# Kernel tuning notes

Hardware: AMD Instinct MI355X
Metric: run time of the kernel (lower is better)

Reference implementation:

```python
import jax, jax.numpy as jnp
import numpy as np

DIM = 64      # channels
HEADS = 2     # num_heads -> head_dim = 32
K = 7         # neighborhood kernel_size (hardcoded in module)
B, H, W = 1, 96, 96
STAGES = 3
HEAD_DIM = DIM // HEADS


def setup_inputs() -> dict:
    key = jax.random.key(0)
    ks = jax.random.split(key, 6)
    x = jax.random.normal(ks[0], (B, DIM, H, W), jnp.float32)
    qkv_w = jax.random.normal(ks[1], (STAGES, 3 * DIM, DIM), jnp.float32) * 0.02
    qkv_b = jnp.zeros((STAGES, 3 * DIM), jnp.float32)
    proj_w = jax.random.normal(ks[2], (STAGES, DIM, DIM), jnp.float32) * 0.02
    proj_b = jnp.zeros((STAGES, DIM), jnp.float32)
    rpb = jax.random.normal(ks[3], (STAGES, HEADS, 2 * K - 1, 2 * K - 1), jnp.float32) * 0.02
    return {"x": x, "qkv_w": qkv_w, "qkv_b": qkv_b, "proj_w": proj_w,
            "proj_b": proj_b, "rpb": rpb}


def _window_idx(n):
    # NATTEN-style clamped sliding windows: each query attends to exactly K keys.
    starts = jnp.clip(jnp.arange(n) - K // 2, 0, n - K)
    idx = starts[:, None] + jnp.arange(K)          # [n, K] absolute key positions
    rel = idx - jnp.arange(n)[:, None] + (K - 1)   # [n, K] rpb index in [0, 2K-2]
    return idx, rel


def _na_stage(x, qkv_w, qkv_b, proj_w, proj_b, rpb, prev_attn):
    # x: [B, H, W, C]
    b, h_, w_, c = x.shape
    qkv = x @ qkv_w.T + qkv_b                                    # [B,H,W,3C]
    qkv = qkv.reshape(b, h_, w_, 3, HEADS, HEAD_DIM)
    qkv = jnp.transpose(qkv, (3, 0, 4, 1, 2, 5))                 # [3,B,h,H,W,d]
    q, k, v = qkv[0], qkv[1], qkv[2]
    scale = HEAD_DIM ** -0.5

    idx_h, rel_h = _window_idx(h_)
    idx_w, rel_w = _window_idx(w_)

    def gather_nb(t):  # t: [B,h,H,W,d] -> [B,h,H,W,K*K,d]
        t = t[:, :, idx_h]                       # [B,h,H,K,W,d]
        t = t[:, :, :, :, idx_w]                 # [B,h,H,K,W,K,d]
        t = jnp.transpose(t, (0, 1, 2, 4, 3, 5, 6))  # [B,h,H,W,K,K,d]
        return t.reshape(b, HEADS, h_, w_, K * K, HEAD_DIM)

    k_nb = gather_nb(k)
    v_nb = gather_nb(v)

    attn = jnp.einsum('bhijd,bhijkd->bhijk', q * scale, k_nb)   # [B,h,H,W,K*K]

    # relative positional bias: rpb[head, rel_h, rel_w]
    bias = rpb[:, rel_h[:, :, None, None], rel_w[None, None, :, :]]  # [h,H,K,W,K]
    bias = jnp.transpose(bias, (0, 1, 3, 2, 4)).reshape(HEADS, h_, w_, K * K)
    attn = attn + bias[None]

    if prev_attn is not None:  # high-order chaining: previous attention map added to logits
        attn = attn + prev_attn

    attn = jax.nn.softmax(attn, axis=-1)
    out = jnp.einsum('bhijk,bhijkd->bhijd', attn, v_nb)          # [B,h,H,W,d]
    out = jnp.transpose(out, (0, 2, 3, 1, 4)).reshape(b, h_, w_, c)
    out = out @ proj_w.T + proj_b
    return out, attn


def reference(x, qkv_w, qkv_b, proj_w, proj_b, rpb):
    xh = jnp.transpose(x, (0, 2, 3, 1))  # NCHW -> NHWC
    attn = None
    for s in range(STAGES):
        xh, attn = _na_stage(xh, qkv_w[s], qkv_b[s], proj_w[s], proj_b[s], rpb[s], attn)
    return jnp.transpose(xh, (0, 3, 1, 2))  # NHWC -> NCHW
```

## Files before the change

kernel.cpp:

```cpp
#include <hip/hip_runtime.h>

#define HW 96
#define NPIX 9216
#define QN 192
#define SCALE 0.17677669529663687f
#define NT 576

__device__ __forceinline__ int xswz(int row, int col) {
    return row * 64 + (((col & 60) ^ (((row >> 2) & 7) << 2)) | (col & 3));
}
__device__ __forceinline__ int wswz(int row, int col) {
    return row * 64 + (((col & 60) ^ ((row & 7) << 2)) | (col & 3));
}

template <int PAT>
__device__ __forceinline__ float swzf(float v) {
    return __int_as_float(__builtin_amdgcn_ds_swizzle(__float_as_int(v), PAT));
}

template <int N>
struct PVChain {
    static __device__ __forceinline__ void run(const float* __restrict__ vbase,
                                               const float* __restrict__ wk,
                                               float& a0, float& a1, float& c0, float& c1) {
        PVChain<N - 1>::run(vbase, wk, a0, a1, c0, c1);
        constexpr int kn = N >> 4, ln = N & 15;
        constexpr int av = N / 7, bv = N % 7;
        float w = __int_as_float(__builtin_amdgcn_ds_swizzle(
                      __float_as_int(wk[kn]), (ln << 5) | 0x10));
        const float2 v = *(const float2*)(vbase + (av * HW + bv) * QN);
        if (N & 1) { c0 = fmaf(w, v.x, c0); c1 = fmaf(w, v.y, c1); }
        else       { a0 = fmaf(w, v.x, a0); a1 = fmaf(w, v.y, a1); }
    }
};
template <>
struct PVChain<-1> {
    static __device__ __forceinline__ void run(const float*, const float*,
                                               float&, float&, float&, float&) {}
};

__device__ __forceinline__ void qkv_gemm(const float* __restrict__ xs,
                                         const float* __restrict__ ws,
                                         const float* __restrict__ qb,
                                         float* __restrict__ qkv,
                                         int i0, int j0c, int t)
{
    const int pxg = t % 9, jo = t / 9;
    const int jb = jo * 3;
    float acc[2][3];
    #pragma unroll
    for (int jj = 0; jj < 3; ++jj) {
        float bv = qb[jb + jj];
        acc[0][jj] = bv; acc[1][jj] = bv;
    }
    #pragma unroll
    for (int cc = 0; cc < 16; ++cc) {
        float4 xv[2], wv[3];
        #pragma unroll
        for (int ii = 0; ii < 2; ++ii)
            xv[ii] = *(const float4*)&xs[xswz(pxg * 2 + ii, cc * 4)];
        #pragma unroll
        for (int jj = 0; jj < 3; ++jj)
            wv[jj] = *(const float4*)&ws[wswz(jb + jj, cc * 4)];
        #pragma unroll
        for (int ii = 0; ii < 2; ++ii)
            #pragma unroll
            for (int jj = 0; jj < 3; ++jj) {
                acc[ii][jj] = fmaf(xv[ii].x, wv[jj].x, acc[ii][jj]);
                acc[ii][jj] = fmaf(xv[ii].y, wv[jj].y, acc[ii][jj]);
                acc[ii][jj] = fmaf(xv[ii].z, wv[jj].z, acc[ii][jj]);
                acc[ii][jj] = fmaf(xv[ii].w, wv[jj].w, acc[ii][jj]);
            }
    }
    #pragma unroll
    for (int ii = 0; ii < 2; ++ii) {
        int px = pxg * 2 + ii;
        float* o = qkv + ((i0 + px / 3) * HW + j0c + px % 3) * QN + jb;
        o[0] = acc[ii][0]; o[1] = acc[ii][1]; o[2] = acc[ii][2];
    }
}

__global__ __launch_bounds__(NT) void k_qkv0(const float* __restrict__ x,
                                             const float* __restrict__ qw,
                                             const float* __restrict__ qb,
                                             float* __restrict__ qkv)
{
    __shared__ float xs[18 * 64];
    __shared__ float ws[QN * 64];
    const int t = threadIdx.x;
    const int i0 = (blockIdx.x >> 5) * 6, j0c = (blockIdx.x & 31) * 3;
    #pragma unroll
    for (int it = 0; it < 2; ++it) {
        int l = it * NT + t;
        int px = l % 18, c = l / 18;
        xs[xswz(px, c)] = x[c * NPIX + (i0 + px / 3) * HW + j0c + px % 3];
    }
    #pragma unroll
    for (int it = 0; it < 6; ++it) {
        int l = it * NT + t;
        if (l < 3072) {
            int j = l >> 4, cs = (l & 15) << 2;
            *(float4*)&ws[wswz(j, cs)] = *(const float4*)&qw[j * 64 + cs];
        }
    }
    __syncthreads();
    qkv_gemm(xs, ws, qb, qkv, i0, j0c, t);
}

template <int HASPREV, int LAST>
__global__ __launch_bounds__(NT) void k_stage(const float* __restrict__ qkv,
                                              const float* __restrict__ rpb,
                                              const float* __restrict__ prev,
                                              float* __restrict__ cur,
                                              const float* __restrict__ pw,
                                              const float* __restrict__ pb,
                                              const float* __restrict__ qw,
                                              const float* __restrict__ qb,
                                              float* __restrict__ qkvn,
                                              float* __restrict__ outp)
{
    __shared__ float xs[18 * 64];
    __shared__ float ws[QN * 64];
    const int t = threadIdx.x;
    const int i0 = (blockIdx.x >> 5) * 6, j0c = (blockIdx.x & 31) * 3;
    #pragma unroll
    for (int it = 0; it < 2; ++it) {
        int l = it * NT + t;
        if (l < 1024) {
            int j = l >> 4, cs = (l & 15) << 2;
            *(float4*)&ws[wswz(j, cs)] = *(const float4*)&pw[j * 64 + cs];
        }
    }
    const int r = t & 15, g = t >> 4;
    const int h = g & 1, pl = g >> 1;
    const int i = i0 + pl / 3, jx = j0c + pl % 3;
    const int p = i * HW + jx;
    int si = i - 3;  si = si < 0 ? 0 : (si > 89 ? 89 : si);
    int sj = jx - 3; sj = sj < 0 ? 0 : (sj > 89 ? 89 : sj);
    float4 q[8];
    {
        const float4* qp = (const float4*)(qkv + p * QN + h * 32);
        #pragma unroll
        for (int d = 0; d < 8; ++d) q[d] = qp[d];
    }
    float pr[4] = {0.f, 0.f, 0.f, 0.f};
    if (HASPREV) {
        float4 z = *(const float4*)(prev + (p * 2 + h) * 64 + r * 4);
        pr[0] = z.x; pr[1] = z.y; pr[2] = z.z; pr[3] = z.w;
    }
    const float* kbase = qkv + (si * HW + sj) * QN + 64 + h * 32;
    float lg[4];
    int aa[4], bb[4];
    #pragma unroll
    for (int k = 0; k < 4; ++k) {
        int n = (k << 4) | r;
        int a = (n * 147) >> 10;
        int b = n - a * 7;
        aa[k] = a; bb[k] = b;
        const float4* kp = (const float4*)(kbase + (a * HW + b) * QN);
        float s0 = 0.f, s1 = 0.f, s2 = 0.f, s3 = 0.f;
        #pragma unroll
        for (int d = 0; d < 8; ++d) {
            float4 kv = kp[d];
            s0 = fmaf(q[d].x, kv.x, s0);
            s1 = fmaf(q[d].y, kv.y, s1);
            s2 = fmaf(q[d].z, kv.z, s2);
            s3 = fmaf(q[d].w, kv.w, s3);
        }
        lg[k] = (s0 + s1) + (s2 + s3);
    }
    {
        const float* rp = rpb + h * 169;
        const int rh0 = si - i + 6, rw0 = sj - jx + 6;
        #pragma unroll
        for (int k = 0; k < 4; ++k) {
            int n = (k << 4) | r;
            float v = fmaf(lg[k], SCALE, rp[(rh0 + aa[k]) * 13 + rw0 + bb[k]] + pr[k]);
            lg[k] = (n <= 48) ? v : -1e30f;
        }
    }
    float mx = fmaxf(fmaxf(lg[0], lg[1]), fmaxf(lg[2], lg[3]));
    mx = fmaxf(mx, swzf<0x041F>(mx));
    mx = fmaxf(mx, swzf<0x081F>(mx));
    mx = fmaxf(mx, swzf<0x101F>(mx));
    mx = fmaxf(mx, swzf<0x201F>(mx));
    float wk[4];
    float sum = 0.f;
    #pragma unroll
    for (int k = 0; k < 4; ++k) { wk[k] = expf(lg[k] - mx); sum += wk[k]; }
    sum += swzf<0x041F>(sum);
    sum += swzf<0x081F>(sum);
    sum += swzf<0x101F>(sum);
    sum += swzf<0x201F>(sum);
    const float inv = 1.f / sum;
    wk[0] *= inv; wk[1] *= inv; wk[2] *= inv; wk[3] *= inv;
    if (!LAST)
        *(float4*)(cur + (p * 2 + h) * 64 + r * 4) = make_float4(wk[0], wk[1], wk[2], wk[3]);
    {
        const float* vbase = qkv + (si * HW + sj) * QN + 128 + h * 32 + r * 2;
        float a0 = 0.f, a1 = 0.f, c0 = 0.f, c1 = 0.f;
        PVChain<48>::run(vbase, wk, a0, a1, c0, c1);
        *(float2*)&xs[xswz(pl, h * 32 + r * 2)] = make_float2(a0 + c0, a1 + c1);
    }
    __syncthreads();
    const int pxg = t % 9, jo = t / 9;
    float pa0 = pb[jo], pa1 = pa0;
    #pragma unroll
    for (int cc = 0; cc < 16; ++cc) {
        float4 xv0 = *(const float4*)&xs[xswz(pxg * 2, cc * 4)];
        float4 xv1 = *(const float4*)&xs[xswz(pxg * 2 + 1, cc * 4)];
        float4 wv  = *(const float4*)&ws[wswz(jo, cc * 4)];
        pa0 = fmaf(xv0.x, wv.x, pa0); pa0 = fmaf(xv0.y, wv.y, pa0);
        pa0 = fmaf(xv0.z, wv.z, pa0); pa0 = fmaf(xv0.w, wv.w, pa0);
        pa1 = fmaf(xv1.x, wv.x, pa1); pa1 = fmaf(xv1.y, wv.y, pa1);
        pa1 = fmaf(xv1.z, wv.z, pa1); pa1 = fmaf(xv1.w, wv.w, pa1);
    }
    __syncthreads();
    xs[xswz(pxg * 2, jo)]     = pa0;
    xs[xswz(pxg * 2 + 1, jo)] = pa1;
    if (!LAST) {
        #pragma unroll
        for (int it = 0; it < 6; ++it) {
            int l = it * NT + t;
            if (l < 3072) {
                int j = l >> 4, cs = (l & 15) << 2;
                *(float4*)&ws[wswz(j, cs)] = *(const float4*)&qw[j * 64 + cs];
            }
        }
    }
    __syncthreads();
    if (LAST) {
        #pragma unroll
        for (int it = 0; it < 2; ++it) {
            int l = it * NT + t;
            int px = l % 18, c = l / 18;
            outp[c * NPIX + (i0 + px / 3) * HW + j0c + px % 3] = xs[xswz(px, c)];
        }
        return;
    }
    qkv_gemm(xs, ws, qb, qkvn, i0, j0c, t);
}

extern "C" void kernel_launch(void* const* d_in, const int* in_sizes, int n_in,
                              void* d_out, int out_size, void* d_ws, size_t ws_size,
                              hipStream_t stream)
{
    const float* x   = (const float*)d_in[0];
    const float* qw  = (const float*)d_in[1];
    const float* qb  = (const float*)d_in[2];
    const float* pw  = (const float*)d_in[3];
    const float* pb  = (const float*)d_in[4];
    const float* rpb = (const float*)d_in[5];
    float* out = (float*)d_out;
    float* ws  = (float*)d_ws;

    float* qkvA = ws;
    float* qkvB = qkvA + 1769472;
    float* attA = qkvB + 1769472;
    float* attB = attA + 1179648;

    k_qkv0<<<512, NT, 0, stream>>>(x, qw, qb, qkvA);
    k_stage<0, 0><<<512, NT, 0, stream>>>(qkvA, rpb,       nullptr, attA,
                                          pw,        pb,       qw + 12288, qb + 192, qkvB, nullptr);
    k_stage<1, 0><<<512, NT, 0, stream>>>(qkvB, rpb + 338, attA,    attB,
                                          pw + 4096, pb + 64,  qw + 24576, qb + 384, qkvA, nullptr);
    k_stage<1, 1><<<512, NT, 0, stream>>>(qkvA, rpb + 676, attB,    nullptr,
                                          pw + 8192, pb + 128, nullptr,    nullptr,  nullptr, out);
}
```

Baseline: 185.7 us.

## Stage Q and attention weights in LDS, compact attention map stride

Loads Q for the block cooperatively into shared memory and computes the four logits per lane in one interleaved loop over head-dim chunks. Softmax weights go to an LDS buffer, which replaces the ds_swizzle broadcast chain in the PV product, and the stored attention map shrinks from 64 to 52 floats per pixel-head. Shuffles replace ds_swizzle for the reductions, and the launch bounds gain an occupancy hint. This adds LDS usage and an extra barrier but cuts global traffic for the prev/cur attention maps and register pressure.

```diff
diff --git a/kernel.cpp b/kernel.cpp
--- a/kernel.cpp
+++ b/kernel.cpp
@@ -3,6 +3,7 @@
 #define HW 96
 #define NPIX 9216
 #define QN 192
+#define ASTRIDE 52
 #define SCALE 0.17677669529663687f
 #define NT 576
 
@@ -12,32 +13,6 @@
 __device__ __forceinline__ int wswz(int row, int col) {
     return row * 64 + (((col & 60) ^ ((row & 7) << 2)) | (col & 3));
 }
-
-template <int PAT>
-__device__ __forceinline__ float swzf(float v) {
-    return __int_as_float(__builtin_amdgcn_ds_swizzle(__float_as_int(v), PAT));
-}
-
-template <int N>
-struct PVChain {
-    static __device__ __forceinline__ void run(const float* __restrict__ vbase,
-                                               const float* __restrict__ wk,
-                                               float& a0, float& a1, float& c0, float& c1) {
-        PVChain<N - 1>::run(vbase, wk, a0, a1, c0, c1);
-        constexpr int kn = N >> 4, ln = N & 15;
-        constexpr int av = N / 7, bv = N % 7;
-        float w = __int_as_float(__builtin_amdgcn_ds_swizzle(
-                      __float_as_int(wk[kn]), (ln << 5) | 0x10));
-        const float2 v = *(const float2*)(vbase + (av * HW + bv) * QN);
-        if (N & 1) { c0 = fmaf(w, v.x, c0); c1 = fmaf(w, v.y, c1); }
-        else       { a0 = fmaf(w, v.x, a0); a1 = fmaf(w, v.y, a1); }
-    }
-};
-template <>
-struct PVChain<-1> {
-    static __device__ __forceinline__ void run(const float*, const float*,
-                                               float&, float&, float&, float&) {}
-};
 
 __device__ __forceinline__ void qkv_gemm(const float* __restrict__ xs,
                                          const float* __restrict__ ws,
@@ -80,10 +55,10 @@
     }
 }
 
-__global__ __launch_bounds__(NT) void k_qkv0(const float* __restrict__ x,
-                                             const float* __restrict__ qw,
-                                             const float* __restrict__ qb,
-                                             float* __restrict__ qkv)
+__global__ __launch_bounds__(NT, 5) void k_qkv0(const float* __restrict__ x,
+                                                const float* __restrict__ qw,
+                                                const float* __restrict__ qb,
+                                                float* __restrict__ qkv)
 {
     __shared__ float xs[18 * 64];
     __shared__ float ws[QN * 64];
@@ -108,19 +83,21 @@
 }
 
 template <int HASPREV, int LAST>
-__global__ __launch_bounds__(NT) void k_stage(const float* __restrict__ qkv,
-                                              const float* __restrict__ rpb,
-                                              const float* __restrict__ prev,
-                                              float* __restrict__ cur,
-                                              const float* __restrict__ pw,
-                                              const float* __restrict__ pb,
-                                              const float* __restrict__ qw,
-                                              const float* __restrict__ qb,
-                                              float* __restrict__ qkvn,
-                                              float* __restrict__ outp)
+__global__ __launch_bounds__(NT, 5) void k_stage(const float* __restrict__ qkv,
+                                                 const float* __restrict__ rpb,
+                                                 const float* __restrict__ prev,
+                                                 float* __restrict__ cur,
+                                                 const float* __restrict__ pw,
+                                                 const float* __restrict__ pb,
+                                                 const float* __restrict__ qw,
+                                                 const float* __restrict__ qb,
+                                                 float* __restrict__ qkvn,
+                                                 float* __restrict__ outp)
 {
     __shared__ float xs[18 * 64];
     __shared__ float ws[QN * 64];
+    __shared__ float qs_s[36 * 32];
+    __shared__ float att_s[36 * 52];
     const int t = threadIdx.x;
     const int i0 = (blockIdx.x >> 5) * 6, j0c = (blockIdx.x & 31) * 3;
     #pragma unroll
@@ -131,76 +108,113 @@
             *(float4*)&ws[wswz(j, cs)] = *(const float4*)&pw[j * 64 + cs];
         }
     }
-    const int r = t & 15, g = t >> 4;
+    if (t < 288) {
+        int gq = t >> 3, dc = t & 7;
+        int hq = gq & 1, plq = gq >> 1;
+        int pq = (i0 + plq / 3) * HW + j0c + plq % 3;
+        *(float4*)&qs_s[gq * 32 + dc * 4] =
+            *(const float4*)&qkv[pq * QN + hq * 32 + dc * 4];
+    }
+    __syncthreads();
+    const int ln = t & 15, g = t >> 4;
     const int h = g & 1, pl = g >> 1;
     const int i = i0 + pl / 3, jx = j0c + pl % 3;
     const int p = i * HW + jx;
     int si = i - 3;  si = si < 0 ? 0 : (si > 89 ? 89 : si);
     int sj = jx - 3; sj = sj < 0 ? 0 : (sj > 89 ? 89 : sj);
-    float4 q[8];
-    {
-        const float4* qp = (const float4*)(qkv + p * QN + h * 32);
-        #pragma unroll
-        for (int d = 0; d < 8; ++d) q[d] = qp[d];
-    }
-    float pr[4] = {0.f, 0.f, 0.f, 0.f};
-    if (HASPREV) {
-        float4 z = *(const float4*)(prev + (p * 2 + h) * 64 + r * 4);
-        pr[0] = z.x; pr[1] = z.y; pr[2] = z.z; pr[3] = z.w;
-    }
-    const float* kbase = qkv + (si * HW + sj) * QN + 64 + h * 32;
-    float lg[4];
+    const float* kb = qkv + (si * HW + sj) * QN + 64 + h * 32;
+    const float* kp[4];
     int aa[4], bb[4];
     #pragma unroll
     for (int k = 0; k < 4; ++k) {
-        int n = (k << 4) | r;
+        int n = (k << 4) | ln;
         int a = (n * 147) >> 10;
         int b = n - a * 7;
         aa[k] = a; bb[k] = b;
-        const float4* kp = (const float4*)(kbase + (a * HW + b) * QN);
-        float s0 = 0.f, s1 = 0.f, s2 = 0.f, s3 = 0.f;
-        #pragma unroll
-        for (int d = 0; d < 8; ++d) {
-            float4 kv = kp[d];
-            s0 = fmaf(q[d].x, kv.x, s0);
-            s1 = fmaf(q[d].y, kv.y, s1);
-            s2 = fmaf(q[d].z, kv.z, s2);
-            s3 = fmaf(q[d].w, kv.w, s3);
-        }
-        lg[k] = (s0 + s1) + (s2 + s3);
-    }
+        kp[k] = kb + (a * HW + b) * QN;
+    }
+    float s0 = 0.f, s1 = 0.f, s2 = 0.f, s3 = 0.f;
+    #pragma unroll
+    for (int dc = 0; dc < 8; ++dc) {
+        float4 qv = *(const float4*)&qs_s[g * 32 + dc * 4];
+        float4 k0 = *(const float4*)&kp[0][dc * 4];
+        float4 k1 = *(const float4*)&kp[1][dc * 4];
+        float4 k2 = *(const float4*)&kp[2][dc * 4];
+        float4 k3 = *(const float4*)&kp[3][dc * 4];
+        s0 = fmaf(qv.x, k0.x, s0); s0 = fmaf(qv.y, k0.y, s0);
+        s0 = fmaf(qv.z, k0.z, s0); s0 = fmaf(qv.w, k0.w, s0);
+        s1 = fmaf(qv.x, k1.x, s1); s1 = fmaf(qv.y, k1.y, s1);
+        s1 = fmaf(qv.z, k1.z, s1); s1 = fmaf(qv.w, k1.w, s1);
+        s2 = fmaf(qv.x, k2.x, s2); s2 = fmaf(qv.y, k2.y, s2);
+        s2 = fmaf(qv.z, k2.z, s2); s2 = fmaf(qv.w, k2.w, s2);
+        s3 = fmaf(qv.x, k3.x, s3); s3 = fmaf(qv.y, k3.y, s3);
+        s3 = fmaf(qv.z, k3.z, s3); s3 = fmaf(qv.w, k3.w, s3);
+    }
+    float lg[4] = {s0, s1, s2, s3};
     {
         const float* rp = rpb + h * 169;
-        const int rh0 = si - i + 6, rw0 = sj - jx + 6;
+        const int rbase = (si - i + 6) * 13 + (sj - jx + 6);
+        const int gp = p * 2 + h;
         #pragma unroll
         for (int k = 0; k < 4; ++k) {
-            int n = (k << 4) | r;
-            float v = fmaf(lg[k], SCALE, rp[(rh0 + aa[k]) * 13 + rw0 + bb[k]] + pr[k]);
-            lg[k] = (n <= 48) ? v : -1e30f;
+            int n = (k << 4) | ln;
+            int ok = (n <= 48);
+            int bidx = ok ? (rbase + aa[k] * 13 + bb[k]) : 0;
+            float bv = rp[bidx];
+            float pv = 0.f;
+            if (HASPREV) pv = prev[gp * ASTRIDE + (ok ? n : 0)];
+            float l2 = fmaf(lg[k], SCALE, bv + pv);
+            lg[k] = ok ? l2 : -1e30f;
         }
     }
     float mx = fmaxf(fmaxf(lg[0], lg[1]), fmaxf(lg[2], lg[3]));
-    mx = fmaxf(mx, swzf<0x041F>(mx));
-    mx = fmaxf(mx, swzf<0x081F>(mx));
-    mx = fmaxf(mx, swzf<0x101F>(mx));
-    mx = fmaxf(mx, swzf<0x201F>(mx));
+    mx = fmaxf(mx, __shfl_xor(mx, 1));
+    mx = fmaxf(mx, __shfl_xor(mx, 2));
+    mx = fmaxf(mx, __shfl_xor(mx, 4));
+    mx = fmaxf(mx, __shfl_xor(mx, 8));
     float wk[4];
     float sum = 0.f;
     #pragma unroll
     for (int k = 0; k < 4; ++k) { wk[k] = expf(lg[k] - mx); sum += wk[k]; }
-    sum += swzf<0x041F>(sum);
-    sum += swzf<0x081F>(sum);
-    sum += swzf<0x101F>(sum);
-    sum += swzf<0x201F>(sum);
+    sum += __shfl_xor(sum, 1);
+    sum += __shfl_xor(sum, 2);
+    sum += __shfl_xor(sum, 4);
+    sum += __shfl_xor(sum, 8);
     const float inv = 1.f / sum;
     wk[0] *= inv; wk[1] *= inv; wk[2] *= inv; wk[3] *= inv;
-    if (!LAST)
-        *(float4*)(cur + (p * 2 + h) * 64 + r * 4) = make_float4(wk[0], wk[1], wk[2], wk[3]);
+    att_s[g * ASTRIDE + ln]      = wk[0];
+    att_s[g * ASTRIDE + 16 + ln] = wk[1];
+    att_s[g * ASTRIDE + 32 + ln] = wk[2];
+    if (ln == 0) att_s[g * ASTRIDE + 48] = wk[3];
     {
-        const float* vbase = qkv + (si * HW + sj) * QN + 128 + h * 32 + r * 2;
-        float a0 = 0.f, a1 = 0.f, c0 = 0.f, c1 = 0.f;
-        PVChain<48>::run(vbase, wk, a0, a1, c0, c1);
-        *(float2*)&xs[xswz(pl, h * 32 + r * 2)] = make_float2(a0 + c0, a1 + c1);
+        const float* vb = qkv + (si * HW + sj) * QN + 128 + h * 32 + ln * 2;
+        float a0 = 0.f, a1 = 0.f;
+        #pragma unroll
+        for (int kk = 0; kk < 12; ++kk) {
+            float4 w4 = *(const float4*)&att_s[g * ASTRIDE + kk * 4];
+            #pragma unroll
+            for (int c = 0; c < 4; ++c) {
+                int n = kk * 4 + c;
+                int a = n / 7, b = n % 7;
+                float w = (&w4.x)[c];
+                float2 v = *(const float2*)&vb[(a * HW + b) * QN];
+                a0 = fmaf(w, v.x, a0); a1 = fmaf(w, v.y, a1);
+            }
+        }
+        {
+            float w = att_s[g * ASTRIDE + 48];
+            float2 v = *(const float2*)&vb[(6 * HW + 6) * QN];
+            a0 = fmaf(w, v.x, a0); a1 = fmaf(w, v.y, a1);
+        }
+        *(float2*)&xs[xswz(pl, h * 32 + ln * 2)] = make_float2(a0, a1);
+    }
+    if (!LAST) {
+        const int gp = p * 2 + h;
+        if (ln < 12)
+            *(float4*)&cur[gp * ASTRIDE + ln * 4] =
+                *(const float4*)&att_s[g * ASTRIDE + ln * 4];
+        else if (ln == 12)
+            cur[gp * ASTRIDE + 48] = att_s[g * ASTRIDE + 48];
     }
     __syncthreads();
     const int pxg = t % 9, jo = t / 9;
@@ -257,7 +271,7 @@
     float* qkvA = ws;
     float* qkvB = qkvA + 1769472;
     float* attA = qkvB + 1769472;
-    float* attB = attA + 1179648;
+    float* attB = attA + 958464;
 
     k_qkv0<<<512, NT, 0, stream>>>(x, qw, qb, qkvA);
     k_stage<0, 0><<<512, NT, 0, stream>>>(qkvA, rpb,       nullptr, attA,
```

Result: slower. 285.7 us (+53.8%).
